# Kernel tuning notes

Hardware: AMD Instinct MI355X
Metric: run time of the kernel (lower is better)

The kernel has to match this reference:

```python
import jax, jax.numpy as jnp
import numpy as np
import itertools

K = 10            # knn size in GFM
SHARP = 20.0      # GMCCE_Sharp
THRES = 0.5       # GMCCE_Thres
EPS = 1e-6
P_EPS = 1e-7      # procrustes epsilon
_COMB = np.array(list(itertools.combinations(range(K), 2)))  # (45,2)


def _tri_areas_sorted(pcd, tri):
    # pcd: (B,N,3) points; tri: (B,N,P,3) int vertex indices -> (B,N,P,3)
    g = jax.vmap(lambda p, t: p[t])(pcd, tri)        # (B,N,P,3,3)
    e1 = g[..., 1, :] - g[..., 0, :]
    e2 = g[..., 2, :] - g[..., 0, :]
    areas = 0.5 * jnp.linalg.norm(jnp.cross(e1, e2), axis=-1)  # (B,N,P)
    z = jnp.zeros_like(areas)
    # original stores area in channel 0 of a zero (.,.,.,3) buffer then sorts ascending
    return jnp.sort(jnp.stack([areas, z, z], axis=-1), axis=-1)


def _gfm(src, tgt):
    # src: (B,3,N); tgt: (B,N,3) -> 0/1 weights (B,N)
    B, _, N = src.shape
    p = jnp.swapaxes(src, 1, 2)                       # (B,N,3)
    sq = jnp.sum(p * p, axis=-1)
    d2 = sq[:, :, None] + sq[:, None, :] - 2.0 * jnp.einsum('bnd,bmd->bnm', p, p)
    w = jnp.exp(-jnp.maximum(d2, 0.0) / 2.0)          # sigma=1; cdist**2 == d2
    _, knn_idx = jax.lax.top_k(w, K)                  # (B,N,K) nearest (incl. self)
    pairs = knn_idx[:, :, _COMB]                      # (B,N,45,2)
    n_p = _COMB.shape[0]
    self_idx = jnp.broadcast_to(jnp.arange(N)[None, :, None, None], (B, N, n_p, 1))
    tri = jnp.concatenate([self_idx, pairs], axis=-1) # (B,N,45,3)
    sl = _tri_areas_sorted(p, tri)
    tl = _tri_areas_sorted(tgt, tri) + EPS
    loss = jnp.sum((sl - tl) ** 2, axis=-1) / jnp.sum(sl + tl, axis=-1)  # (B,N,45)
    sorted_loss = jnp.sort(loss, axis=-1)
    reg = jnp.linalg.norm(sl - tl, axis=-1)
    total = sorted_loss + 0.1 * reg
    med = jnp.median(total, axis=-1, keepdims=True)
    total = jnp.where(total > 3.0 * med, 0.0, total)
    limited = jnp.sqrt(total[:, :, :K] + EPS)
    mean_loss = jnp.mean(limited, axis=-1)            # (B,N)
    min_loss = jnp.min(mean_loss, axis=-1, keepdims=True)
    wts = 2.0 * jax.nn.sigmoid(-SHARP * (mean_loss - min_loss))
    return jnp.where(wts > THRES, 1.0, 0.0)


def _procrustes(X, Y, w):
    # X,Y: (N,3); w: (N,1) weights (detached in original)
    tw = jnp.sum(jnp.abs(w))
    nw = jnp.broadcast_to(w.reshape(-1, 1), X.shape) / (tw + P_EPS)
    mx = jnp.sum(nw * X, axis=0, keepdims=True)       # (1,3)
    my = jnp.sum(nw * Y, axis=0, keepdims=True)
    cov = (Y - my).T @ (nw * (X - mx))                # (3,3)
    U, _, Vh = jnp.linalg.svd(cov)
    sign = jnp.where(jnp.linalg.det(U) * jnp.linalg.det(Vh) < 0, -1.0, 1.0)
    S = jnp.diag(jnp.stack([jnp.ones(()), jnp.ones(()), sign]))
    R = U @ S @ Vh
    # faithful to original: (3,) - (3,1) broadcasts to (3,3)
    T = my.reshape(3) - R @ mx.T
    return R, T


def setup_inputs() -> dict:
    key = jax.random.key(0)
    k1, k2, k3, k4, k5 = jax.random.split(key, 5)
    B, D, N = 8, 512, 2048
    return {
        'src_embedding': jax.random.normal(k1, (B, D, N), dtype=jnp.float32),
        'tgt_embedding': jax.random.normal(k2, (B, D, N), dtype=jnp.float32),
        'src': jax.random.normal(k3, (B, 3, N), dtype=jnp.float32),
        'tgt': jax.random.normal(k4, (B, 3, N), dtype=jnp.float32),
        'temperature': jax.random.uniform(k5, (B, 1), dtype=jnp.float32),
        'is_corr': 1,
    }


def reference(src_embedding, tgt_embedding, src, tgt, temperature, is_corr):
    d_k = src_embedding.shape[1]
    scores = jnp.einsum('bdn,bdm->bnm', src_embedding, tgt_embedding) / jnp.sqrt(jnp.float32(d_k))
    scores = jax.nn.softmax(10000.0 * scores, axis=2)  # (B,N,N)
    corres = jnp.argmax(scores, axis=-1)               # (B,N)
    tgt_t = jnp.swapaxes(tgt, 1, 2)                    # (B,N,3)
    src_t = jnp.swapaxes(src, 1, 2)
    corr_tgt = jnp.einsum('bnm,bmd->bnd', scores, tgt_t)
    weight = _gfm(src, corr_tgt)[..., None]            # (B,N,1)
    src_corr = jnp.take_along_axis(tgt_t, corres[..., None], axis=1)  # (B,N,3)
    R, T = jax.vmap(_procrustes)(src_t, src_corr, jax.lax.stop_gradient(weight))
    return R, T, corres[..., None], weight
```

## Files before the change

kernel.cpp:

```cpp
#include <hip/hip_runtime.h>
#include <math.h>

#define BATCH 8
#define DIM   512
#define NPTS  2048
#define KNN   10
#define NPAIR 45
#define KCAP  64

typedef __attribute__((ext_vector_type(8))) short    bf16x8;
typedef __attribute__((ext_vector_type(4))) float    f32x4;
typedef __attribute__((ext_vector_type(4))) unsigned int u32x4;

__device__ inline unsigned short bf16_rne(float x) {
    unsigned int u = __float_as_uint(x);
    u += 0x7FFFu + ((u >> 16) & 1u);
    return (unsigned short)(u >> 16);
}
__device__ inline float bf16_to_f(unsigned short h) {
    return __uint_as_float(((unsigned int)h) << 16);
}
__device__ inline unsigned long long shflx_u64(unsigned long long v, int mask) {
    unsigned int lo = (unsigned int)v, hi = (unsigned int)(v >> 32);
    lo = (unsigned int)__shfl_xor((int)lo, mask);
    hi = (unsigned int)__shfl_xor((int)hi, mask);
    return ((unsigned long long)hi << 32) | lo;
}

__global__ __launch_bounds__(256)
void split_kernel(const float* __restrict__ se, const float* __restrict__ te,
                  unsigned short* __restrict__ pA, unsigned short* __restrict__ pB)
{
    const int bid = blockIdx.x;
    const int tensor = bid >> 11;
    const int rr_ = bid & 2047;
    const int b  = rr_ >> 8;
    const int dt = (rr_ >> 5) & 7;
    const int nt = rr_ & 31;
    const float* srcp = (tensor == 0 ? se : te)
                        + ((size_t)b * DIM + dt * 64) * NPTS + nt * 64;
    unsigned short* dst = (tensor == 0 ? pA : pB);
    const size_t PL = (size_t)BATCH * NPTS * DIM;
    unsigned short* base = dst + (size_t)b * NPTS * DIM + (size_t)nt * 64 * DIM + dt * 64;

    __shared__ float T[64][65];
    const int t = threadIdx.x;
    {
        int r = t >> 4, c4 = t & 15;
        #pragma unroll
        for (int it = 0; it < 4; ++it) {
            int d = r + it * 16;
            float4 v = *(const float4*)&srcp[(size_t)d * NPTS + c4 * 4];
            T[d][c4 * 4 + 0] = v.x; T[d][c4 * 4 + 1] = v.y;
            T[d][c4 * 4 + 2] = v.z; T[d][c4 * 4 + 3] = v.w;
        }
    }
    __syncthreads();
    const int n  = t >> 2;
    const int d0 = (t & 3) * 16;
    unsigned short hh[16], mm[16], ll[16];
    #pragma unroll
    for (int j = 0; j < 16; ++j) {
        float a = T[d0 + j][n];
        unsigned short h = bf16_rne(a);
        float r1 = a - bf16_to_f(h);
        unsigned short m = bf16_rne(r1);
        float r2 = r1 - bf16_to_f(m);
        unsigned short l = bf16_rne(r2);
        hh[j] = h; mm[j] = m; ll[j] = l;
    }
    unsigned short* o = base + (size_t)n * DIM + d0;
    *(u32x4*)(o)            = *(u32x4*)&hh[0];
    *(u32x4*)(o + 8)        = *(u32x4*)&hh[8];
    *(u32x4*)(o + PL)       = *(u32x4*)&mm[0];
    *(u32x4*)(o + PL + 8)   = *(u32x4*)&mm[8];
    *(u32x4*)(o + 2*PL)     = *(u32x4*)&ll[0];
    *(u32x4*)(o + 2*PL + 8) = *(u32x4*)&ll[8];
}

__global__ __launch_bounds__(256, 2)
void score_h(const unsigned short* __restrict__ pA, const unsigned short* __restrict__ pB,
             unsigned short* __restrict__ uhat)
{
    const int bid  = blockIdx.x;
    const int xcd  = bid & 7;
    const int slot = bid >> 3;
    const int g    = xcd + 8 * (slot >> 4);
    const int ntile = slot & 15;
    const int b    = g >> 2;
    const int mc   = g & 3;
    const int n0 = ntile * 128;
    const int t  = threadIdx.x;
    const int w  = t >> 6;
    const int l  = t & 63;
    const int wn = w >> 1, wm = w & 1;
    const int l15 = l & 15, l4 = l >> 4;

    __shared__ unsigned short As[128 * 64];
    __shared__ unsigned short Bs[128 * 64];

    int srow[4], skg[4], ldsoff[4];
    #pragma unroll
    for (int qq = 0; qq < 4; ++qq) {
        int s = qq * 256 + t;
        int row = s >> 3, slt = s & 7;
        srow[qq] = row;
        skg[qq] = slt ^ (row & 7);
        ldsoff[qq] = row * 64 + slt * 8;
    }
    int aroff[4], arxor[4], broff[4], brxor[4];
    #pragma unroll
    for (int i = 0; i < 4; ++i) {
        int ar = wn * 64 + i * 16 + l15;
        aroff[i] = ar * 64; arxor[i] = ar & 7;
        int br = wm * 64 + i * 16 + l15;
        broff[i] = br * 64; brxor[i] = br & 7;
    }

    const float scl = 10000.0f / sqrtf((float)DIM);
    const unsigned short* Ab = pA + (size_t)b * NPTS * DIM;
    const unsigned short* Bb = pB + (size_t)b * NPTS * DIM;

    for (int mt = 0; mt < 4; ++mt) {
        const int m0 = mc * 512 + mt * 128;
        f32x4 acc[4][4];
        #pragma unroll
        for (int i = 0; i < 4; ++i)
            #pragma unroll
            for (int j = 0; j < 4; ++j) acc[i][j] = (f32x4){0.f, 0.f, 0.f, 0.f};

        for (int k0 = 0; k0 < 512; k0 += 64) {
            __syncthreads();
            bf16x8 ra[4], rb[4];
            #pragma unroll
            for (int qq = 0; qq < 4; ++qq) {
                ra[qq] = *(const bf16x8*)&Ab[(size_t)(n0 + srow[qq]) * DIM + k0 + skg[qq] * 8];
                rb[qq] = *(const bf16x8*)&Bb[(size_t)(m0 + srow[qq]) * DIM + k0 + skg[qq] * 8];
            }
            #pragma unroll
            for (int qq = 0; qq < 4; ++qq) {
                *(bf16x8*)&As[ldsoff[qq]] = ra[qq];
                *(bf16x8*)&Bs[ldsoff[qq]] = rb[qq];
            }
            __syncthreads();
            #pragma unroll
            for (int ks = 0; ks < 2; ++ks) {
                bf16x8 af[4], bfr[4];
                #pragma unroll
                for (int i = 0; i < 4; ++i) {
                    af[i]  = *(const bf16x8*)&As[aroff[i] + (((ks * 4 + l4) ^ arxor[i]) * 8)];
                    bfr[i] = *(const bf16x8*)&Bs[broff[i] + (((ks * 4 + l4) ^ brxor[i]) * 8)];
                }
                #pragma unroll
                for (int i = 0; i < 4; ++i)
                    #pragma unroll
                    for (int j = 0; j < 4; ++j)
                        acc[i][j] = __builtin_amdgcn_mfma_f32_16x16x32_bf16(af[i], bfr[j], acc[i][j], 0, 0, 0);
            }
        }
        #pragma unroll
        for (int i = 0; i < 4; ++i) {
            #pragma unroll
            for (int j = 0; j < 4; ++j) {
                int mcol = m0 + wm * 64 + j * 16 + l15;
                #pragma unroll
                for (int r = 0; r < 4; ++r) {
                    int nabs = n0 + wn * 64 + i * 16 + l4 * 4 + r;
                    uhat[((size_t)(b * NPTS + nabs)) * NPTS + mcol] =
                        bf16_rne(scl * acc[i][j][r]);
                }
            }
        }
    }
}

__global__ __launch_bounds__(256)
void resolve(const unsigned short* __restrict__ uhat,
             const unsigned short* __restrict__ pA, const unsigned short* __restrict__ pB,
             const float* __restrict__ tgt,
             float* __restrict__ corr_tgt, int* __restrict__ corres_i,
             float* __restrict__ corres_out)
{
    const int wid  = threadIdx.x >> 6;
    const int lane = threadIdx.x & 63;
    const int gid  = blockIdx.x * 4 + wid;
    const int b    = gid >> 11;
    const int n    = gid & 2047;

    __shared__ int s_m[4][64];
    __shared__ int s_cnt[4];

    if (lane == 0) s_cnt[wid] = 0;
    __syncthreads();

    const unsigned short* urow = uhat + (size_t)gid * NPTS;
    float v[32];
    float lmax = -3.402823466e38f; int lk = 0;
    #pragma unroll
    for (int g2 = 0; g2 < 4; ++g2) {
        u32x4 pk = *(const u32x4*)&urow[lane * 32 + g2 * 8];
        #pragma unroll
        for (int e = 0; e < 4; ++e) {
            unsigned int w2 = pk[e];
            float f0 = __uint_as_float((w2 & 0xFFFFu) << 16);
            float f1 = __uint_as_float(w2 & 0xFFFF0000u);
            int k0 = g2 * 8 + e * 2;
            v[k0] = f0; v[k0 + 1] = f1;
            if (f0 > lmax) { lmax = f0; lk = k0; }
            if (f1 > lmax) { lmax = f1; lk = k0 + 1; }
        }
    }
    float vmax = lmax; int argm = lane * 32 + lk;
    #pragma unroll
    for (int mask = 1; mask < 64; mask <<= 1) {
        float ov = __shfl_xor(vmax, mask);
        int   oi = __shfl_xor(argm, mask);
        if (ov > vmax || (ov == vmax && oi < argm)) { vmax = ov; argm = oi; }
    }
    const float cut = vmax - 1200.0f;
    int cnt2 = 0;
    #pragma unroll
    for (int k = 0; k < 32; ++k) cnt2 += (v[k] >= cut) ? 1 : 0;
    int nc = cnt2;
    #pragma unroll
    for (int mask = 1; mask < 64; mask <<= 1) nc += __shfl_xor(nc, mask);

    if (nc > 1) {
        #pragma unroll
        for (int k = 0; k < 32; ++k) {
            if (v[k] >= cut) {
                int slot = atomicAdd(&s_cnt[wid], 1);
                if (slot < 64) s_m[wid][slot] = lane * 32 + k;
            }
        }
    }
    __syncthreads();
    if (nc > 1 && lane == 0) {
        int ncc = nc > 64 ? 64 : nc;
        for (int i = 1; i < ncc; ++i) {
            int key = s_m[wid][i]; int j = i - 1;
            while (j >= 0 && s_m[wid][j] > key) { s_m[wid][j + 1] = s_m[wid][j]; --j; }
            s_m[wid][j + 1] = key;
        }
    }
    __syncthreads();

    if (nc == 1) {
        if (lane < 3) corr_tgt[(size_t)gid * 3 + lane] = tgt[((size_t)b * 3 + lane) * NPTS + argm];
        if (lane == 0) { corres_i[gid] = argm; corres_out[gid] = (float)argm; }
        return;
    }
    const int ncc = nc > 64 ? 64 : nc;

    const size_t PL = (size_t)BATCH * NPTS * DIM;
    const unsigned short* Ar = pA + ((size_t)b * NPTS + n) * DIM + lane * 8;
    bf16x8 a_h = *(const bf16x8*)&Ar[0];
    bf16x8 a_m = *(const bf16x8*)&Ar[PL];
    bf16x8 a_l = *(const bf16x8*)&Ar[2 * PL];
    float ah[8], am[8], al[8];
    #pragma unroll
    for (int e = 0; e < 8; ++e) {
        ah[e] = bf16_to_f((unsigned short)a_h[e]);
        am[e] = bf16_to_f((unsigned short)a_m[e]);
        al[e] = bf16_to_f((unsigned short)a_l[e]);
    }

    const float sqd = sqrtf((float)DIM);
    float umax = -3.402823466e38f; int uarg = 0x7fffffff;
    float myu = 0.f;
    for (int c = 0; c < ncc; ++c) {
        int mB = s_m[wid][c];
        const unsigned short* Br = pB + ((size_t)b * NPTS + mB) * DIM + lane * 8;
        bf16x8 b_h = *(const bf16x8*)&Br[0];
        bf16x8 b_m = *(const bf16x8*)&Br[PL];
        bf16x8 b_l = *(const bf16x8*)&Br[2 * PL];
        float part = 0.f;
        #pragma unroll
        for (int e = 0; e < 8; ++e) {
            float bh = bf16_to_f((unsigned short)b_h[e]);
            float bm = bf16_to_f((unsigned short)b_m[e]);
            float bl = bf16_to_f((unsigned short)b_l[e]);
            part += ah[e] * bh;
            part += ah[e] * bm;
            part += am[e] * bh;
            part += ah[e] * bl;
            part += am[e] * bm;
            part += al[e] * bh;
        }
        #pragma unroll
        for (int mask = 1; mask < 64; mask <<= 1) part += __shfl_xor(part, mask);
        float u = 10000.0f * (part / sqd);
        if (u > umax) { umax = u; uarg = mB; }
        if (lane == c) myu = u;
    }

    float p = (lane < ncc) ? expf(myu - umax) : 0.f;
    int myM = (lane < ncc) ? s_m[wid][lane] : 0;
    float tx = 0.f, ty = 0.f, tz = 0.f, ps = p;
    if (lane < ncc) {
        tx = p * tgt[((size_t)b * 3 + 0) * NPTS + myM];
        ty = p * tgt[((size_t)b * 3 + 1) * NPTS + myM];
        tz = p * tgt[((size_t)b * 3 + 2) * NPTS + myM];
    }
    #pragma unroll
    for (int mask = 1; mask < 64; mask <<= 1) {
        ps += __shfl_xor(ps, mask);
        tx += __shfl_xor(tx, mask);
        ty += __shfl_xor(ty, mask);
        tz += __shfl_xor(tz, mask);
    }
    if (lane == 0) {
        corr_tgt[(size_t)gid * 3 + 0] = tx / ps;
        corr_tgt[(size_t)gid * 3 + 1] = ty / ps;
        corr_tgt[(size_t)gid * 3 + 2] = tz / ps;
        corres_i[gid]   = uarg;
        corres_out[gid] = (float)uarg;
    }
}

__global__ __launch_bounds__(256, 2)
void score_mfma(const unsigned short* __restrict__ pA, const unsigned short* __restrict__ pB,
                const float* __restrict__ tgt, float* __restrict__ part)
{
    const int bid  = blockIdx.x;
    const int xcd  = bid & 7;
    const int slot = bid >> 3;
    const int g    = xcd + 8 * (slot >> 4);
    const int ntile = slot & 15;
    const int b    = g >> 2;
    const int mc   = g & 3;
    const int n0 = ntile * 128;
    const int t  = threadIdx.x;
    const int w  = t >> 6;
    const int l  = t & 63;
    const int wn = w >> 1, wm = w & 1;
    const int l15 = l & 15, l4 = l >> 4;

    __shared__ unsigned short As[128 * 64];
    __shared__ unsigned short Bs[128 * 64];

    const size_t PL = (size_t)BATCH * NPTS * DIM;

    int srow[4], skg[4], ldsoff[4];
    #pragma unroll
    for (int qq = 0; qq < 4; ++qq) {
        int s = qq * 256 + t;
        int row = s >> 3, slt = s & 7;
        srow[qq] = row;
        skg[qq] = slt ^ (row & 7);
        ldsoff[qq] = row * 64 + slt * 8;
    }
    int aroff[4], arxor[4], broff[4], brxor[4];
    #pragma unroll
    for (int i = 0; i < 4; ++i) {
        int ar = wn * 64 + i * 16 + l15;
        aroff[i] = ar * 64; arxor[i] = ar & 7;
        int br = wm * 64 + i * 16 + l15;
        broff[i] = br * 64; brxor[i] = br & 7;
    }

    float mx[16], sm[16], ax[16], ay[16], az[16]; int ag[16];
    #pragma unroll
    for (int si = 0; si < 16; ++si) {
        mx[si] = -3.402823466e38f; sm[si] = 0.f;
        ax[si] = 0.f; ay[si] = 0.f; az[si] = 0.f; ag[si] = 0;
    }

    const float sqd = sqrtf((float)DIM);
    const unsigned short* Ab = pA + (size_t)b * NPTS * DIM;
    const unsigned short* Bb = pB + (size_t)b * NPTS * DIM;
    const int AIDX[6] = {0, 0, 1, 0, 1, 2};
    const int BIDX[6] = {0, 1, 0, 2, 1, 0};

    for (int mt = 0; mt < 4; ++mt) {
        const int m0 = mc * 512 + mt * 128;
        f32x4 acc[4][4];
        #pragma unroll
        for (int i = 0; i < 4; ++i)
            #pragma unroll
            for (int j = 0; j < 4; ++j) acc[i][j] = (f32x4){0.f, 0.f, 0.f, 0.f};

        for (int q = 0; q < 6; ++q) {
            const unsigned short* Ap = Ab + (size_t)AIDX[q] * PL;
            const unsigned short* Bp = Bb + (size_t)BIDX[q] * PL;
            for (int k0 = 0; k0 < 512; k0 += 64) {
                __syncthreads();
                bf16x8 ra[4], rb[4];
                #pragma unroll
                for (int qq = 0; qq < 4; ++qq) {
                    ra[qq] = *(const bf16x8*)&Ap[(size_t)(n0 + srow[qq]) * DIM + k0 + skg[qq] * 8];
                    rb[qq] = *(const bf16x8*)&Bp[(size_t)(m0 + srow[qq]) * DIM + k0 + skg[qq] * 8];
                }
                #pragma unroll
                for (int qq = 0; qq < 4; ++qq) {
                    *(bf16x8*)&As[ldsoff[qq]] = ra[qq];
                    *(bf16x8*)&Bs[ldsoff[qq]] = rb[qq];
                }
                __syncthreads();
                #pragma unroll
                for (int ks = 0; ks < 2; ++ks) {
                    bf16x8 af[4], bfr[4];
                    #pragma unroll
                    for (int i = 0; i < 4; ++i) {
                        af[i]  = *(const bf16x8*)&As[aroff[i] + (((ks * 4 + l4) ^ arxor[i]) * 8)];
                        bfr[i] = *(const bf16x8*)&Bs[broff[i] + (((ks * 4 + l4) ^ brxor[i]) * 8)];
                    }
                    #pragma unroll
                    for (int i = 0; i < 4; ++i)
                        #pragma unroll
                        for (int j = 0; j < 4; ++j)
                            acc[i][j] = __builtin_amdgcn_mfma_f32_16x16x32_bf16(af[i], bfr[j], acc[i][j], 0, 0, 0);
                }
            }
        }
        float tg0[4], tg1[4], tg2[4];
        #pragma unroll
        for (int j = 0; j < 4; ++j) {
            int mcol = m0 + wm * 64 + j * 16 + l15;
            tg0[j] = tgt[((size_t)b * 3 + 0) * NPTS + mcol];
            tg1[j] = tgt[((size_t)b * 3 + 1) * NPTS + mcol];
            tg2[j] = tgt[((size_t)b * 3 + 2) * NPTS + mcol];
        }
        #pragma unroll
        for (int i = 0; i < 4; ++i) {
            #pragma unroll
            for (int r = 0; r < 4; ++r) {
                const int si = i * 4 + r;
                float u[4];
                float lm = -3.402823466e38f; int la = 0;
                #pragma unroll
                for (int j = 0; j < 4; ++j) {
                    float s  = acc[i][j][r] / sqd;
                    float uu = 10000.0f * s;
                    u[j] = uu;
                    if (uu > lm) { lm = uu; la = m0 + wm * 64 + j * 16 + l15; }
                }
                float nm = fmaxf(mx[si], lm);
                if (lm > mx[si]) ag[si] = la;
                float f = expf(mx[si] - nm);
                mx[si] = nm;
                float s_ = sm[si] * f, x_ = ax[si] * f, y_ = ay[si] * f, z_ = az[si] * f;
                #pragma unroll
                for (int j = 0; j < 4; ++j) {
                    float p = expf(u[j] - nm);
                    s_ += p; x_ += p * tg0[j]; y_ += p * tg1[j]; z_ += p * tg2[j];
                }
                sm[si] = s_; ax[si] = x_; ay[si] = y_; az[si] = z_;
            }
        }
    }

    #pragma unroll
    for (int si = 0; si < 16; ++si) {
        for (int mask = 1; mask < 16; mask <<= 1) {
            float omx = __shfl_xor(mx[si], mask);
            float osm = __shfl_xor(sm[si], mask);
            float oax = __shfl_xor(ax[si], mask);
            float oay = __shfl_xor(ay[si], mask);
            float oaz = __shfl_xor(az[si], mask);
            int   oag = __shfl_xor(ag[si], mask);
            float nm = fmaxf(mx[si], omx);
            float f1 = expf(mx[si] - nm), f2 = expf(omx - nm);
            sm[si] = sm[si] * f1 + osm * f2;
            ax[si] = ax[si] * f1 + oax * f2;
            ay[si] = ay[si] * f1 + oay * f2;
            az[si] = az[si] * f1 + oaz * f2;
            ag[si] = (omx > mx[si]) ? oag : ((omx == mx[si]) ? min(ag[si], oag) : ag[si]);
            mx[si] = nm;
        }
    }
    if (l15 == 0) {
        const int chunk = mc * 2 + wm;
        #pragma unroll
        for (int i = 0; i < 4; ++i)
            #pragma unroll
            for (int r = 0; r < 4; ++r) {
                const int si = i * 4 + r;
                int nabs = n0 + wn * 64 + i * 16 + l4 * 4 + r;
                size_t o = (((size_t)b * NPTS + nabs) * 8 + chunk) * 8;
                part[o + 0] = mx[si]; part[o + 1] = sm[si];
                part[o + 2] = ax[si]; part[o + 3] = ay[si]; part[o + 4] = az[si];
                part[o + 5] = __int_as_float(ag[si]);
            }
    }
}

__global__ __launch_bounds__(256)
void merge8_kernel(const float* __restrict__ part, float* __restrict__ corr_tgt,
                   int* __restrict__ corres_i, float* __restrict__ corres_out)
{
    int r = blockIdx.x * 256 + threadIdx.x;
    float m = -3.402823466e38f, s = 0.f, x = 0.f, y = 0.f, z = 0.f; int a = 0x7fffffff;
    for (int c = 0; c < 8; ++c) {
        const float* p = &part[((size_t)r * 8 + c) * 8];
        float pm = p[0]; int pa = __float_as_int(p[5]);
        float nm = fmaxf(m, pm);
        float f1 = expf(m - nm), f2 = expf(pm - nm);
        s = s * f1 + p[1] * f2;
        x = x * f1 + p[2] * f2;
        y = y * f1 + p[3] * f2;
        z = z * f1 + p[4] * f2;
        if (pm > m) a = pa; else if (pm == m) a = min(a, pa);
        m = nm;
    }
    corr_tgt[(size_t)r * 3 + 0] = x / s;
    corr_tgt[(size_t)r * 3 + 1] = y / s;
    corr_tgt[(size_t)r * 3 + 2] = z / s;
    corres_i[r]   = a;
    corres_out[r] = (float)a;
}

__global__ __launch_bounds__(256)
void prep_p4(const float* __restrict__ src, float4* __restrict__ P4)
{
    int i = blockIdx.x * 256 + threadIdx.x;
    int b = i >> 11, m = i & 2047;
    float x = src[((size_t)b * 3 + 0) * NPTS + m];
    float y = src[((size_t)b * 3 + 1) * NPTS + m];
    float z = src[((size_t)b * 3 + 2) * NPTS + m];
    P4[i] = make_float4(x, y, z, x * x + y * y + z * z);
}

__global__ __launch_bounds__(256)
void knn_topk(const float4* __restrict__ P4, int* __restrict__ topI)
{
    const int bid = blockIdx.x;
    const int b = bid >> 8, nblk = bid & 255;
    const int t = threadIdx.x;
    const int c  = t & 31;
    const int rl = t >> 5;
    const int n = nblk * 8 + rl;
    const float4* Pb = P4 + (size_t)b * NPTS;
    const float4 pn = Pb[n];

    __shared__ unsigned long long Lbuf[8][KCAP];
    __shared__ int cnt[8];
    if (c == 0) cnt[rl] = 0;
    __syncthreads();

    float lmin = 3.402823466e38f;
    for (int i = 0; i < 64; ++i) {
        int m = i * 32 + c;
        float4 pm = Pb[m];
        float dot = pn.x * pm.x + pn.y * pm.y + pn.z * pm.z;
        float d2 = (pn.w + pm.w) - 2.0f * dot;
        d2 = fmaxf(d2, 0.f);
        lmin = fminf(lmin, d2);
    }
    float vv = lmin, Tt = 0.f;
    for (int r = 0; r < 10; ++r) {
        float gm = vv;
        #pragma unroll
        for (int mask = 1; mask < 32; mask <<= 1)
            gm = fminf(gm, __shfl_xor(gm, mask));
        Tt = gm;
        vv = (vv == gm) ? 3.402823466e38f : vv;
    }
    const float Tp = Tt + 1e-4f;

    for (int i = 0; i < 64; ++i) {
        int m = i * 32 + c;
        float4 pm = Pb[m];
        float dot = pn.x * pm.x + pn.y * pm.y + pn.z * pm.z;
        float d2 = (pn.w + pm.w) - 2.0f * dot;
        d2 = fmaxf(d2, 0.f);
        if (d2 <= Tp) {
            float w = expf(-d2 * 0.5f);
            unsigned long long key =
                ((unsigned long long)(~__float_as_uint(w)) << 32) | (unsigned int)m;
            int slot = atomicAdd(&cnt[rl], 1);
            if (slot < KCAP) Lbuf[rl][slot] = key;
        }
    }
    __syncthreads();

    unsigned long long kl[KNN];
    const int cr = cnt[rl];
    if (cr <= KCAP) {
        const unsigned long long UMAX = 0xFFFFFFFFFFFFFFFFull;
        unsigned long long e0 = (c      < cr) ? Lbuf[rl][c]      : UMAX;
        unsigned long long e1 = (c + 32 < cr) ? Lbuf[rl][c + 32] : UMAX;
        kl[0] = e0 < e1 ? e0 : e1;
        kl[1] = e0 < e1 ? e1 : e0;
        #pragma unroll
        for (int k = 2; k < KNN; ++k) kl[k] = UMAX;
    } else {
        unsigned int kx[KNN], ix[KNN];
        #pragma unroll
        for (int k = 0; k < KNN; ++k) { kx[k] = 0xFFFFFFFFu; ix[k] = 0xFFFFFFFFu; }
        for (int i = 0; i < 64; ++i) {
            int m = i * 32 + c;
            float4 pm = Pb[m];
            float dot = pn.x * pm.x + pn.y * pm.y + pn.z * pm.z;
            float d2 = (pn.w + pm.w) - 2.0f * dot;
            d2 = fmaxf(d2, 0.f);
            float w = expf(-d2 * 0.5f);
            unsigned int key = ~__float_as_uint(w);
            if (key < kx[KNN - 1]) {
                unsigned int ck = key, ci = (unsigned int)m;
                #pragma unroll
                for (int k = 0; k < KNN; ++k) {
                    bool lt = ck < kx[k];
                    unsigned int tk = kx[k], ti = ix[k];
                    kx[k] = lt ? ck : kx[k];
                    ix[k] = lt ? ci : ix[k];
                    ck = lt ? tk : ck;
                    ci = lt ? ti : ci;
                }
            }
        }
        #pragma unroll
        for (int k = 0; k < KNN; ++k)
            kl[k] = ((unsigned long long)kx[k] << 32) | ix[k];
    }

    #pragma unroll
    for (int mask = 1; mask < 32; mask <<= 1) {
        unsigned long long B[KNN];
        #pragma unroll
        for (int k = 0; k < KNN; ++k) B[k] = shflx_u64(kl[k], mask);
        unsigned long long M[KNN];
        #pragma unroll
        for (int k = 0; k < KNN; ++k) {
            unsigned long long best = B[k];
            #pragma unroll
            for (int i = 1; i <= k; ++i) {
                unsigned long long hi = kl[i - 1] > B[k - i] ? kl[i - 1] : B[k - i];
                best = hi < best ? hi : best;
            }
            unsigned long long ak = kl[k];
            M[k] = ak < best ? ak : best;
        }
        #pragma unroll
        for (int k = 0; k < KNN; ++k) kl[k] = M[k];
    }

    if (c == 0) {
        size_t gid = (size_t)(b << 11) + n;
        #pragma unroll
        for (int k = 0; k < KNN; ++k)
            topI[gid * KNN + k] = (int)(kl[k] & 0xFFFFFFFFull);
    }
}

__global__ __launch_bounds__(256)
void gfm_finish(const float4* __restrict__ P4, const float* __restrict__ corr_tgt,
                const int* __restrict__ topI, float* __restrict__ mean_loss)
{
    const int wid  = threadIdx.x >> 6;
    const int lane = threadIdx.x & 63;
    const int gid  = blockIdx.x * 4 + wid;
    const int b    = gid >> 11;

    __shared__ float PT[4][KNN][6];
    __shared__ float LS[4][48];
    __shared__ float SR[4][48];
    __shared__ float TOT[4][48];

    if (lane < KNN) {
        int idx = topI[(size_t)gid * KNN + lane];
        float4 pk = P4[(b << 11) + idx];
        size_t o = ((size_t)(b << 11) + idx) * 3;
        PT[wid][lane][0] = pk.x; PT[wid][lane][1] = pk.y; PT[wid][lane][2] = pk.z;
        PT[wid][lane][3] = corr_tgt[o];
        PT[wid][lane][4] = corr_tgt[o + 1];
        PT[wid][lane][5] = corr_tgt[o + 2];
    }
    float4 pn = P4[gid];
    size_t on = (size_t)gid * 3;
    const float cnx = corr_tgt[on], cny = corr_tgt[on + 1], cnz = corr_tgt[on + 2];
    __syncthreads();

    int pi = 0, pj = 1;
    {
        int pp = lane;
        #pragma unroll
        for (int r = 0; r < 9; ++r) {
            int cnt3 = 9 - r;
            if (pp >= 0 && pp < cnt3) { pi = r; pj = r + 1 + pp; }
            pp -= cnt3;
        }
    }

    float ls_p = 0.f, rg_p = 0.f;
    if (lane < NPAIR) {
        float e1x = PT[wid][pi][0] - pn.x, e1y = PT[wid][pi][1] - pn.y, e1z = PT[wid][pi][2] - pn.z;
        float e2x = PT[wid][pj][0] - pn.x, e2y = PT[wid][pj][1] - pn.y, e2z = PT[wid][pj][2] - pn.z;
        float cx = e1y * e2z - e1z * e2y;
        float cy = e1z * e2x - e1x * e2z;
        float cz = e1x * e2y - e1y * e2x;
        float as_ = 0.5f * sqrtf(cx * cx + cy * cy + cz * cz);
        float f1x = PT[wid][pi][3] - cnx, f1y = PT[wid][pi][4] - cny, f1z = PT[wid][pi][5] - cnz;
        float f2x = PT[wid][pj][3] - cnx, f2y = PT[wid][pj][4] - cny, f2z = PT[wid][pj][5] - cnz;
        float gx = f1y * f2z - f1z * f2y;
        float gy = f1z * f2x - f1x * f2z;
        float gz = f1x * f2y - f1y * f2x;
        float at_ = 0.5f * sqrtf(gx * gx + gy * gy + gz * gz);
        float tl2 = at_ + 1e-6f;
        float dd  = as_ - tl2;
        float e2_ = 1e-6f * 1e-6f;
        float num = (e2_ + e2_) + dd * dd;
        float den = (1e-6f + 1e-6f) + (as_ + tl2);
        ls_p = num / den;
        rg_p = sqrtf(num);
        LS[wid][lane] = ls_p;
    }
    __syncthreads();

    int rk = 0;
    if (lane < NPAIR) {
        #pragma unroll
        for (int q = 0; q < NPAIR; ++q) {
            float lq = LS[wid][q];
            rk += (lq < ls_p) || (lq == ls_p && q < lane);
        }
        SR[wid][rk] = ls_p;
    }
    __syncthreads();

    float tot_p = 0.f;
    if (lane < NPAIR) {
        tot_p = SR[wid][lane] + 0.1f * rg_p;
        TOT[wid][lane] = tot_p;
    }
    __syncthreads();

    int rt2 = 0;
    if (lane < NPAIR) {
        #pragma unroll
        for (int q = 0; q < NPAIR; ++q) {
            float tq = TOT[wid][q];
            rt2 += (tq < tot_p) || (tq == tot_p && q < lane);
        }
        SR[wid][rt2] = tot_p;
    }
    __syncthreads();

    float med = SR[wid][22];
    float thr = 3.0f * med;
    if (lane < KNN) {
        float v = tot_p;
        v = (v > thr) ? 0.0f : v;
        LS[wid][lane] = sqrtf(v + 1e-6f);
    }
    __syncthreads();
    if (lane == 0) {
        float acc = 0.f;
        #pragma unroll
        for (int k = 0; k < KNN; ++k) acc += LS[wid][k];
        mean_loss[gid] = acc / 10.0f;
    }
}

__global__ __launch_bounds__(256)
void weight_kernel(const float* __restrict__ mean_loss, float* __restrict__ weight_out)
{
    const int b = blockIdx.x;
    const int t = threadIdx.x;
    __shared__ float red[256];
    float mn = 3.402823466e38f;
    for (int i = t; i < NPTS; i += 256)
        mn = fminf(mn, mean_loss[(size_t)b * NPTS + i]);
    red[t] = mn; __syncthreads();
    for (int s2 = 128; s2 > 0; s2 >>= 1) {
        if (t < s2) red[t] = fminf(red[t], red[t + s2]);
        __syncthreads();
    }
    float ml = red[0];
    for (int i = t; i < NPTS; i += 256) {
        float d = mean_loss[(size_t)b * NPTS + i] - ml;
        float e = expf(-20.0f * d);
        float wts = 2.0f * (e / (1.0f + e));
        weight_out[(size_t)b * NPTS + i] = (wts > 0.5f) ? 1.0f : 0.0f;
    }
}

__device__ void jacobi4(double A[4][4], double V[4][4]) {
    for (int i = 0; i < 4; ++i)
        for (int j = 0; j < 4; ++j) V[i][j] = (i == j) ? 1.0 : 0.0;
    for (int sweep = 0; sweep < 12; ++sweep) {
        for (int p = 0; p < 3; ++p) for (int q = p + 1; q < 4; ++q) {
            double apq = A[p][q];
            if (fabs(apq) < 1e-30) continue;
            double theta = (A[q][q] - A[p][p]) / (2.0 * apq);
            double tt = (theta >= 0 ? 1.0 : -1.0) / (fabs(theta) + sqrt(theta * theta + 1.0));
            double c = 1.0 / sqrt(tt * tt + 1.0), s = tt * c;
            for (int k = 0; k < 4; ++k) {
                double akp = A[k][p], akq = A[k][q];
                A[k][p] = c * akp - s * akq;
                A[k][q] = s * akp + c * akq;
            }
            for (int k = 0; k < 4; ++k) {
                double apk = A[p][k], aqk = A[q][k];
                A[p][k] = c * apk - s * aqk;
                A[q][k] = s * apk + c * aqk;
            }
            for (int k = 0; k < 4; ++k) {
                double vkp = V[k][p], vkq = V[k][q];
                V[k][p] = c * vkp - s * vkq;
                V[k][q] = s * vkp + c * vkq;
            }
        }
    }
}

__global__ __launch_bounds__(256)
void procrustes_kernel(const float* __restrict__ src, const float* __restrict__ tgt,
                       const int* __restrict__ corres_i, const float* __restrict__ weight,
                       float* __restrict__ outR, float* __restrict__ outT)
{
    const int b = blockIdx.x;
    const int t = threadIdx.x;
    __shared__ float red[256][9];
    __shared__ float s_tw, s_mx[3], s_my[3];
    __shared__ float s_cov[9];

    float a0 = 0, a1 = 0, a2 = 0, a3 = 0, a4 = 0, a5 = 0, a6 = 0;
    for (int i = t; i < NPTS; i += 256) {
        float w = weight[(size_t)b * NPTS + i];
        float X0 = src[((size_t)b * 3 + 0) * NPTS + i];
        float X1 = src[((size_t)b * 3 + 1) * NPTS + i];
        float X2 = src[((size_t)b * 3 + 2) * NPTS + i];
        int c = corres_i[(size_t)b * NPTS + i];
        float Y0 = tgt[((size_t)b * 3 + 0) * NPTS + c];
        float Y1 = tgt[((size_t)b * 3 + 1) * NPTS + c];
        float Y2 = tgt[((size_t)b * 3 + 2) * NPTS + c];
        a0 += w;
        a1 += w * X0; a2 += w * X1; a3 += w * X2;
        a4 += w * Y0; a5 += w * Y1; a6 += w * Y2;
    }
    red[t][0] = a0; red[t][1] = a1; red[t][2] = a2; red[t][3] = a3;
    red[t][4] = a4; red[t][5] = a5; red[t][6] = a6; red[t][7] = 0; red[t][8] = 0;
    __syncthreads();
    for (int s2 = 128; s2 > 0; s2 >>= 1) {
        if (t < s2)
            for (int k = 0; k < 7; ++k) red[t][k] += red[t + s2][k];
        __syncthreads();
    }
    if (t == 0) {
        float tw = red[0][0];
        float itw = tw + 1e-7f;
        s_tw = tw;
        s_mx[0] = red[0][1] / itw; s_mx[1] = red[0][2] / itw; s_mx[2] = red[0][3] / itw;
        s_my[0] = red[0][4] / itw; s_my[1] = red[0][5] / itw; s_my[2] = red[0][6] / itw;
    }
    __syncthreads();
    const float twp = s_tw + 1e-7f;
    const float mx0 = s_mx[0], mx1 = s_mx[1], mx2 = s_mx[2];
    const float my0 = s_my[0], my1 = s_my[1], my2 = s_my[2];

    float cv[9] = {0,0,0,0,0,0,0,0,0};
    for (int i = t; i < NPTS; i += 256) {
        float w = weight[(size_t)b * NPTS + i];
        float nwn = w / twp;
        float X0 = src[((size_t)b * 3 + 0) * NPTS + i] - mx0;
        float X1 = src[((size_t)b * 3 + 1) * NPTS + i] - mx1;
        float X2 = src[((size_t)b * 3 + 2) * NPTS + i] - mx2;
        int c = corres_i[(size_t)b * NPTS + i];
        float Y0 = tgt[((size_t)b * 3 + 0) * NPTS + c] - my0;
        float Y1 = tgt[((size_t)b * 3 + 1) * NPTS + c] - my1;
        float Y2 = tgt[((size_t)b * 3 + 2) * NPTS + c] - my2;
        float b0 = nwn * X0, b1 = nwn * X1, b2 = nwn * X2;
        cv[0] += Y0 * b0; cv[1] += Y0 * b1; cv[2] += Y0 * b2;
        cv[3] += Y1 * b0; cv[4] += Y1 * b1; cv[5] += Y1 * b2;
        cv[6] += Y2 * b0; cv[7] += Y2 * b1; cv[8] += Y2 * b2;
    }
    __syncthreads();
    for (int k = 0; k < 9; ++k) red[t][k] = cv[k];
    __syncthreads();
    for (int s2 = 128; s2 > 0; s2 >>= 1) {
        if (t < s2)
            for (int k = 0; k < 9; ++k) red[t][k] += red[t + s2][k];
        __syncthreads();
    }
    if (t == 0) for (int k = 0; k < 9; ++k) s_cov[k] = red[0][k];
    __syncthreads();

    if (t == 0) {
        double cov[3][3];
        for (int i = 0; i < 3; ++i)
            for (int j = 0; j < 3; ++j) cov[i][j] = (double)s_cov[i * 3 + j];
        double S[3][3];
        for (int a = 0; a < 3; ++a)
            for (int bb = 0; bb < 3; ++bb) S[a][bb] = cov[bb][a];
        double N4[4][4];
        N4[0][0] = S[0][0] + S[1][1] + S[2][2];
        N4[0][1] = S[1][2] - S[2][1];
        N4[0][2] = S[2][0] - S[0][2];
        N4[0][3] = S[0][1] - S[1][0];
        N4[1][1] = S[0][0] - S[1][1] - S[2][2];
        N4[1][2] = S[0][1] + S[1][0];
        N4[1][3] = S[2][0] + S[0][2];
        N4[2][2] = -S[0][0] + S[1][1] - S[2][2];
        N4[2][3] = S[1][2] + S[2][1];
        N4[3][3] = -S[0][0] - S[1][1] + S[2][2];
        N4[1][0] = N4[0][1]; N4[2][0] = N4[0][2]; N4[3][0] = N4[0][3];
        N4[2][1] = N4[1][2]; N4[3][1] = N4[1][3]; N4[3][2] = N4[2][3];
        double V[4][4];
        jacobi4(N4, V);
        int best = 0; double bl = N4[0][0];
        for (int k = 1; k < 4; ++k) if (N4[k][k] > bl) { bl = N4[k][k]; best = k; }
        double q0 = V[0][best], qx = V[1][best], qy = V[2][best], qz = V[3][best];
        double nq = sqrt(q0 * q0 + qx * qx + qy * qy + qz * qz);
        q0 /= nq; qx /= nq; qy /= nq; qz /= nq;
        double Rm[3][3];
        Rm[0][0] = q0*q0 + qx*qx - qy*qy - qz*qz;
        Rm[0][1] = 2.0 * (qx*qy - q0*qz);
        Rm[0][2] = 2.0 * (qx*qz + q0*qy);
        Rm[1][0] = 2.0 * (qx*qy + q0*qz);
        Rm[1][1] = q0*q0 - qx*qx + qy*qy - qz*qz;
        Rm[1][2] = 2.0 * (qy*qz - q0*qx);
        Rm[2][0] = 2.0 * (qx*qz - q0*qy);
        Rm[2][1] = 2.0 * (qy*qz + q0*qx);
        Rm[2][2] = q0*q0 - qx*qx - qy*qy + qz*qz;
        double o1 = 0, o2 = 0;
        for (int i = 0; i < 3; ++i)
            for (int j = 0; j < 3; ++j) { o1 += Rm[i][j] * cov[i][j]; o2 += Rm[j][i] * cov[i][j]; }
        if (o2 > o1) {
            for (int i = 0; i < 3; ++i)
                for (int j = i + 1; j < 3; ++j) {
                    double tv = Rm[i][j]; Rm[i][j] = Rm[j][i]; Rm[j][i] = tv;
                }
        }
        float Rf[3][3];
        for (int i = 0; i < 3; ++i)
            for (int j = 0; j < 3; ++j) {
                Rf[i][j] = (float)Rm[i][j];
                outR[(size_t)b * 9 + i * 3 + j] = Rf[i][j];
            }
        float rm[3];
        float mxv[3] = {mx0, mx1, mx2};
        float myv[3] = {my0, my1, my2};
        for (int i = 0; i < 3; ++i)
            rm[i] = Rf[i][0] * mxv[0] + Rf[i][1] * mxv[1] + Rf[i][2] * mxv[2];
        for (int i = 0; i < 3; ++i)
            for (int j = 0; j < 3; ++j)
                outT[(size_t)b * 9 + i * 3 + j] = myv[j] - rm[i];
    }
}

extern "C" void kernel_launch(void* const* d_in, const int* in_sizes, int n_in,
                              void* d_out, int out_size, void* d_ws, size_t ws_size,
                              hipStream_t stream)
{
    const float* se  = (const float*)d_in[0];
    const float* te  = (const float*)d_in[1];
    const float* src = (const float*)d_in[2];
    const float* tgt = (const float*)d_in[3];

    float* out  = (float*)d_out;
    float* outR = out;
    float* outT = out + 72;
    float* outC = out + 144;
    float* outW = out + 144 + BATCH * NPTS;

    char* wsb = (char*)d_ws;
    float* corr_tgt  = (float*)wsb;
    int*   corres_i  = (int*)(wsb + 196608);
    float* mean_loss = (float*)(wsb + 262144);
    float* part      = (float*)(wsb + 327680);

    float4* P4   = (float4*)(wsb + 327680);
    int*    topI = (int*)(wsb + 589824);

    const size_t PLANES_OFF = 4521984;
    const size_t PL_BYTES   = (size_t)3 * BATCH * NPTS * DIM * 2;
    const size_t NEED       = PLANES_OFF + 2 * PL_BYTES;
    const size_t UHAT_BYTES = (size_t)BATCH * NPTS * NPTS * 2;
    const size_t NEED2      = NEED + UHAT_BYTES;

    unsigned short* pA = (unsigned short*)(wsb + PLANES_OFF);
    unsigned short* pB = (unsigned short*)(wsb + PLANES_OFF + PL_BYTES);
    unsigned short* uhat = (unsigned short*)(wsb + NEED);

    hipLaunchKernelGGL(split_kernel, dim3(4096), dim3(256), 0, stream, se, te, pA, pB);
    if (ws_size >= NEED2) {
        hipLaunchKernelGGL(score_h, dim3(512), dim3(256), 0, stream, pA, pB, uhat);
        hipLaunchKernelGGL(resolve, dim3(BATCH * NPTS / 4), dim3(256), 0, stream,
                           uhat, pA, pB, tgt, corr_tgt, corres_i, outC);
    } else {
        hipLaunchKernelGGL(score_mfma, dim3(512), dim3(256), 0, stream, pA, pB, tgt, part);
        hipLaunchKernelGGL(merge8_kernel, dim3(BATCH * NPTS / 256), dim3(256), 0, stream,
                           part, corr_tgt, corres_i, outC);
    }
    hipLaunchKernelGGL(prep_p4, dim3(BATCH * NPTS / 256), dim3(256), 0, stream, src, P4);
    hipLaunchKernelGGL(knn_topk, dim3(BATCH * 256), dim3(256), 0, stream, P4, topI);
    hipLaunchKernelGGL(gfm_finish, dim3(BATCH * NPTS / 4), dim3(256), 0, stream,
                       P4, corr_tgt, topI, mean_loss);
    hipLaunchKernelGGL(weight_kernel, dim3(BATCH), dim3(256), 0, stream,
                       mean_loss, outW);
    hipLaunchKernelGGL(procrustes_kernel, dim3(BATCH), dim3(256), 0, stream,
                       src, tgt, corres_i, outW, outR, outT);
}
```

Measured before the change: 231.2 us.

## Fuse score GEMM and kNN top-k into one heterogeneous kernel launch

Merges the bf16 MFMA score kernel and the kNN top-k kernel into a single launch where every fifth block runs the score tile and the rest run kNN rows. prep_p4 is moved earlier so its output is ready. The aim is to overlap the compute-bound matrix work with the latency-bound kNN work and drop a serial kernel boundary. The kNN blocks now reserve the larger 32KB shared buffer and inherit the score path's launch bounds, which may reduce occupancy for those blocks.

```diff
diff --git a/kernel.cpp b/kernel.cpp
--- a/kernel.cpp
+++ b/kernel.cpp
@@ -78,13 +78,14 @@
     *(u32x4*)(o + 2*PL + 8) = *(u32x4*)&ll[8];
 }
 
-__global__ __launch_bounds__(256, 2)
-void score_h(const unsigned short* __restrict__ pA, const unsigned short* __restrict__ pB,
-             unsigned short* __restrict__ uhat)
-{
-    const int bid  = blockIdx.x;
-    const int xcd  = bid & 7;
-    const int slot = bid >> 3;
+__device__ __forceinline__
+void score_h_body(int sid, const unsigned short* __restrict__ pA,
+                  const unsigned short* __restrict__ pB,
+                  unsigned short* __restrict__ uhat,
+                  unsigned short* As, unsigned short* Bs)
+{
+    const int xcd  = sid & 7;
+    const int slot = sid >> 3;
     const int g    = xcd + 8 * (slot >> 4);
     const int ntile = slot & 15;
     const int b    = g >> 2;
@@ -95,9 +96,6 @@
     const int l  = t & 63;
     const int wn = w >> 1, wm = w & 1;
     const int l15 = l & 15, l4 = l >> 4;
-
-    __shared__ unsigned short As[128 * 64];
-    __shared__ unsigned short Bs[128 * 64];
 
     int srow[4], skg[4], ldsoff[4];
     #pragma unroll
@@ -171,6 +169,145 @@
                 }
             }
         }
+    }
+}
+
+__device__ __forceinline__
+void knn_body(int kid, const float4* __restrict__ P4, int* __restrict__ topI,
+              unsigned long long* Lraw, int* cnt)
+{
+    const int b = kid >> 8, nblk = kid & 255;
+    const int t = threadIdx.x;
+    const int c  = t & 31;
+    const int rl = t >> 5;
+    const int n = nblk * 8 + rl;
+    const float4* Pb = P4 + (size_t)b * NPTS;
+    const float4 pn = Pb[n];
+    unsigned long long* Lbuf = Lraw + rl * KCAP;
+
+    if (c == 0) cnt[rl] = 0;
+    __syncthreads();
+
+    float lmin = 3.402823466e38f;
+    for (int i = 0; i < 64; ++i) {
+        int m = i * 32 + c;
+        float4 pm = Pb[m];
+        float dot = pn.x * pm.x + pn.y * pm.y + pn.z * pm.z;
+        float d2 = (pn.w + pm.w) - 2.0f * dot;
+        d2 = fmaxf(d2, 0.f);
+        lmin = fminf(lmin, d2);
+    }
+    float vv = lmin, Tt = 0.f;
+    for (int r = 0; r < 10; ++r) {
+        float gm = vv;
+        #pragma unroll
+        for (int mask = 1; mask < 32; mask <<= 1)
+            gm = fminf(gm, __shfl_xor(gm, mask));
+        Tt = gm;
+        vv = (vv == gm) ? 3.402823466e38f : vv;
+    }
+    const float Tp = Tt + 1e-4f;
+
+    for (int i = 0; i < 64; ++i) {
+        int m = i * 32 + c;
+        float4 pm = Pb[m];
+        float dot = pn.x * pm.x + pn.y * pm.y + pn.z * pm.z;
+        float d2 = (pn.w + pm.w) - 2.0f * dot;
+        d2 = fmaxf(d2, 0.f);
+        if (d2 <= Tp) {
+            float w = expf(-d2 * 0.5f);
+            unsigned long long key =
+                ((unsigned long long)(~__float_as_uint(w)) << 32) | (unsigned int)m;
+            int slot = atomicAdd(&cnt[rl], 1);
+            if (slot < KCAP) Lbuf[slot] = key;
+        }
+    }
+    __syncthreads();
+
+    unsigned long long kl[KNN];
+    const int cr = cnt[rl];
+    if (cr <= KCAP) {
+        const unsigned long long UMAX = 0xFFFFFFFFFFFFFFFFull;
+        unsigned long long e0 = (c      < cr) ? Lbuf[c]      : UMAX;
+        unsigned long long e1 = (c + 32 < cr) ? Lbuf[c + 32] : UMAX;
+        kl[0] = e0 < e1 ? e0 : e1;
+        kl[1] = e0 < e1 ? e1 : e0;
+        #pragma unroll
+        for (int k = 2; k < KNN; ++k) kl[k] = UMAX;
+    } else {
+        unsigned int kx[KNN], ix[KNN];
+        #pragma unroll
+        for (int k = 0; k < KNN; ++k) { kx[k] = 0xFFFFFFFFu; ix[k] = 0xFFFFFFFFu; }
+        for (int i = 0; i < 64; ++i) {
+            int m = i * 32 + c;
+            float4 pm = Pb[m];
+            float dot = pn.x * pm.x + pn.y * pm.y + pn.z * pm.z;
+            float d2 = (pn.w + pm.w) - 2.0f * dot;
+            d2 = fmaxf(d2, 0.f);
+            float w = expf(-d2 * 0.5f);
+            unsigned int key = ~__float_as_uint(w);
+            if (key < kx[KNN - 1]) {
+                unsigned int ck = key, ci = (unsigned int)m;
+                #pragma unroll
+                for (int k = 0; k < KNN; ++k) {
+                    bool lt = ck < kx[k];
+                    unsigned int tk = kx[k], ti = ix[k];
+                    kx[k] = lt ? ck : kx[k];
+                    ix[k] = lt ? ci : ix[k];
+                    ck = lt ? tk : ck;
+                    ci = lt ? ti : ci;
+                }
+            }
+        }
+        #pragma unroll
+        for (int k = 0; k < KNN; ++k)
+            kl[k] = ((unsigned long long)kx[k] << 32) | ix[k];
+    }
+
+    #pragma unroll
+    for (int mask = 1; mask < 32; mask <<= 1) {
+        unsigned long long B[KNN];
+        #pragma unroll
+        for (int k = 0; k < KNN; ++k) B[k] = shflx_u64(kl[k], mask);
+        unsigned long long M[KNN];
+        #pragma unroll
+        for (int k = 0; k < KNN; ++k) {
+            unsigned long long best = B[k];
+            #pragma unroll
+            for (int i = 1; i <= k; ++i) {
+                unsigned long long hi = kl[i - 1] > B[k - i] ? kl[i - 1] : B[k - i];
+                best = hi < best ? hi : best;
+            }
+            unsigned long long ak = kl[k];
+            M[k] = ak < best ? ak : best;
+        }
+        #pragma unroll
+        for (int k = 0; k < KNN; ++k) kl[k] = M[k];
+    }
+
+    if (c == 0) {
+        size_t gid = (size_t)(b << 11) + n;
+        #pragma unroll
+        for (int k = 0; k < KNN; ++k)
+            topI[gid * KNN + k] = (int)(kl[k] & 0xFFFFFFFFull);
+    }
+}
+
+__global__ __launch_bounds__(256, 2)
+void fused_score_knn(const unsigned short* __restrict__ pA,
+                     const unsigned short* __restrict__ pB,
+                     unsigned short* __restrict__ uhat,
+                     const float4* __restrict__ P4, int* __restrict__ topI)
+{
+    __shared__ unsigned long long SMEM[4096];
+    __shared__ int s_cnt[8];
+    const int bid = blockIdx.x;
+    if (bid % 5 == 0) {
+        unsigned short* As = (unsigned short*)SMEM;
+        unsigned short* Bs = (unsigned short*)SMEM + 8192;
+        score_h_body(bid / 5, pA, pB, uhat, As, Bs);
+    } else {
+        knn_body(bid - bid / 5 - 1, P4, topI, SMEM, s_cnt);
     }
 }
 
@@ -524,123 +661,9 @@
 __global__ __launch_bounds__(256)
 void knn_topk(const float4* __restrict__ P4, int* __restrict__ topI)
 {
-    const int bid = blockIdx.x;
-    const int b = bid >> 8, nblk = bid & 255;
-    const int t = threadIdx.x;
-    const int c  = t & 31;
-    const int rl = t >> 5;
-    const int n = nblk * 8 + rl;
-    const float4* Pb = P4 + (size_t)b * NPTS;
-    const float4 pn = Pb[n];
-
-    __shared__ unsigned long long Lbuf[8][KCAP];
+    __shared__ unsigned long long Lraw[8 * KCAP];
     __shared__ int cnt[8];
-    if (c == 0) cnt[rl] = 0;
-    __syncthreads();
-
-    float lmin = 3.402823466e38f;
-    for (int i = 0; i < 64; ++i) {
-        int m = i * 32 + c;
-        float4 pm = Pb[m];
-        float dot = pn.x * pm.x + pn.y * pm.y + pn.z * pm.z;
-        float d2 = (pn.w + pm.w) - 2.0f * dot;
-        d2 = fmaxf(d2, 0.f);
-        lmin = fminf(lmin, d2);
-    }
-    float vv = lmin, Tt = 0.f;
-    for (int r = 0; r < 10; ++r) {
-        float gm = vv;
-        #pragma unroll
-        for (int mask = 1; mask < 32; mask <<= 1)
-            gm = fminf(gm, __shfl_xor(gm, mask));
-        Tt = gm;
-        vv = (vv == gm) ? 3.402823466e38f : vv;
-    }
-    const float Tp = Tt + 1e-4f;
-
-    for (int i = 0; i < 64; ++i) {
-        int m = i * 32 + c;
-        float4 pm = Pb[m];
-        float dot = pn.x * pm.x + pn.y * pm.y + pn.z * pm.z;
-        float d2 = (pn.w + pm.w) - 2.0f * dot;
-        d2 = fmaxf(d2, 0.f);
-        if (d2 <= Tp) {
-            float w = expf(-d2 * 0.5f);
-            unsigned long long key =
-                ((unsigned long long)(~__float_as_uint(w)) << 32) | (unsigned int)m;
-            int slot = atomicAdd(&cnt[rl], 1);
-            if (slot < KCAP) Lbuf[rl][slot] = key;
-        }
-    }
-    __syncthreads();
-
-    unsigned long long kl[KNN];
-    const int cr = cnt[rl];
-    if (cr <= KCAP) {
-        const unsigned long long UMAX = 0xFFFFFFFFFFFFFFFFull;
-        unsigned long long e0 = (c      < cr) ? Lbuf[rl][c]      : UMAX;
-        unsigned long long e1 = (c + 32 < cr) ? Lbuf[rl][c + 32] : UMAX;
-        kl[0] = e0 < e1 ? e0 : e1;
-        kl[1] = e0 < e1 ? e1 : e0;
-        #pragma unroll
-        for (int k = 2; k < KNN; ++k) kl[k] = UMAX;
-    } else {
-        unsigned int kx[KNN], ix[KNN];
-        #pragma unroll
-        for (int k = 0; k < KNN; ++k) { kx[k] = 0xFFFFFFFFu; ix[k] = 0xFFFFFFFFu; }
-        for (int i = 0; i < 64; ++i) {
-            int m = i * 32 + c;
-            float4 pm = Pb[m];
-            float dot = pn.x * pm.x + pn.y * pm.y + pn.z * pm.z;
-            float d2 = (pn.w + pm.w) - 2.0f * dot;
-            d2 = fmaxf(d2, 0.f);
-            float w = expf(-d2 * 0.5f);
-            unsigned int key = ~__float_as_uint(w);
-            if (key < kx[KNN - 1]) {
-                unsigned int ck = key, ci = (unsigned int)m;
-                #pragma unroll
-                for (int k = 0; k < KNN; ++k) {
-                    bool lt = ck < kx[k];
-                    unsigned int tk = kx[k], ti = ix[k];
-                    kx[k] = lt ? ck : kx[k];
-                    ix[k] = lt ? ci : ix[k];
-                    ck = lt ? tk : ck;
-                    ci = lt ? ti : ci;
-                }
-            }
-        }
-        #pragma unroll
-        for (int k = 0; k < KNN; ++k)
-            kl[k] = ((unsigned long long)kx[k] << 32) | ix[k];
-    }
-
-    #pragma unroll
-    for (int mask = 1; mask < 32; mask <<= 1) {
-        unsigned long long B[KNN];
-        #pragma unroll
-        for (int k = 0; k < KNN; ++k) B[k] = shflx_u64(kl[k], mask);
-        unsigned long long M[KNN];
-        #pragma unroll
-        for (int k = 0; k < KNN; ++k) {
-            unsigned long long best = B[k];
-            #pragma unroll
-            for (int i = 1; i <= k; ++i) {
-                unsigned long long hi = kl[i - 1] > B[k - i] ? kl[i - 1] : B[k - i];
-                best = hi < best ? hi : best;
-            }
-            unsigned long long ak = kl[k];
-            M[k] = ak < best ? ak : best;
-        }
-        #pragma unroll
-        for (int k = 0; k < KNN; ++k) kl[k] = M[k];
-    }
-
-    if (c == 0) {
-        size_t gid = (size_t)(b << 11) + n;
-        #pragma unroll
-        for (int k = 0; k < KNN; ++k)
-            topI[gid * KNN + k] = (int)(kl[k] & 0xFFFFFFFFull);
-    }
+    knn_body(blockIdx.x, P4, topI, Lraw, cnt);
 }
 
 __global__ __launch_bounds__(256)
@@ -974,17 +997,18 @@
     unsigned short* uhat = (unsigned short*)(wsb + NEED);
 
     hipLaunchKernelGGL(split_kernel, dim3(4096), dim3(256), 0, stream, se, te, pA, pB);
+    hipLaunchKernelGGL(prep_p4, dim3(BATCH * NPTS / 256), dim3(256), 0, stream, src, P4);
     if (ws_size >= NEED2) {
-        hipLaunchKernelGGL(score_h, dim3(512), dim3(256), 0, stream, pA, pB, uhat);
+        hipLaunchKernelGGL(fused_score_knn, dim3(2560), dim3(256), 0, stream,
+                           pA, pB, uhat, P4, topI);
         hipLaunchKernelGGL(resolve, dim3(BATCH * NPTS / 4), dim3(256), 0, stream,
                            uhat, pA, pB, tgt, corr_tgt, corres_i, outC);
     } else {
         hipLaunchKernelGGL(score_mfma, dim3(512), dim3(256), 0, stream, pA, pB, tgt, part);
         hipLaunchKernelGGL(merge8_kernel, dim3(BATCH * NPTS / 256), dim3(256), 0, stream,
                            part, corr_tgt, corres_i, outC);
-    }
-    hipLaunchKernelGGL(prep_p4, dim3(BATCH * NPTS / 256), dim3(256), 0, stream, src, P4);
-    hipLaunchKernelGGL(knn_topk, dim3(BATCH * 256), dim3(256), 0, stream, P4, topI);
+        hipLaunchKernelGGL(knn_topk, dim3(BATCH * 256), dim3(256), 0, stream, P4, topI);
+    }
     hipLaunchKernelGGL(gfm_finish, dim3(BATCH * NPTS / 4), dim3(256), 0, stream,
                        P4, corr_tgt, topI, mean_loss);
     hipLaunchKernelGGL(weight_kernel, dim3(BATCH), dim3(256), 0, stream,
```

Result: slower. 264.2 us (+14.3%).
